# Performance work log

Measured on AMD Instinct MI355X. Metric: run time of the kernel, lower is better.

## Reference

```python
import jax, jax.numpy as jnp
import numpy as np

DIM = 1024
HEADS = 16
HEAD_DIM = DIM // HEADS
SCALE = HEAD_DIM ** -0.5


def setup_inputs() -> dict:
    key = jax.random.key(0)
    ks = jax.random.split(key, 7)
    B, N, M = 2, 2048, 2048
    x = jax.random.normal(ks[0], (B, N, DIM), dtype=jnp.float32)
    y = jax.random.normal(ks[1], (B, M, DIM), dtype=jnp.float32)
    s = DIM ** -0.5
    Wq = jax.random.normal(ks[2], (DIM, DIM), dtype=jnp.float32) * s
    Wk = jax.random.normal(ks[3], (DIM, DIM), dtype=jnp.float32) * s
    Wv = jax.random.normal(ks[4], (DIM, DIM), dtype=jnp.float32) * s
    Wp = jax.random.normal(ks[5], (DIM, DIM), dtype=jnp.float32) * s
    bp = jax.random.normal(ks[6], (DIM,), dtype=jnp.float32) * 0.01
    return {"x": x, "y": y, "Wq": Wq, "Wk": Wk, "Wv": Wv, "Wp": Wp, "bp": bp}


def _split_heads(t):
    b, n, _ = t.shape
    return t.reshape(b, n, HEADS, HEAD_DIM).transpose(0, 2, 1, 3)  # b h n d


def reference(x, y, Wq, Wk, Wv, Wp, bp):
    q = _split_heads(x @ Wq)  # [b,h,n,d]
    k = _split_heads(y @ Wk)  # [b,h,m,d]
    v = _split_heads(y @ Wv)  # [b,h,m,d]
    attn = jnp.einsum('bhid,bhjd->bhij', q, k) * SCALE  # [b,h,n,m]
    attn = jax.nn.softmax(attn, axis=-1)
    out = jnp.einsum('bhij,bhjd->bhid', attn, v)  # [b,h,n,d]
    b, h, n, d = out.shape
    out = out.transpose(0, 2, 1, 3).reshape(b, n, h * d)  # [b,n,dim]
    return out @ Wp + bp
```

## Files before the change

kernel.cpp:

```cpp
#include <hip/hip_runtime.h>
#include <hip/hip_bf16.h>
#include <cstdint>

#define DIM   1024
#define HEADS 16
#define HDIM  64
#define BATCH 2
#define SEQ   2048
#define ROWS  (BATCH*SEQ)
static constexpr float QSCALE = 0.18033688f;

typedef float  f32x4  __attribute__((ext_vector_type(4)));
typedef float  float4v __attribute__((ext_vector_type(4)));
typedef __bf16 bf16x8 __attribute__((ext_vector_type(8)));
typedef __bf16 bf16x4 __attribute__((ext_vector_type(4)));
typedef short  short4v __attribute__((ext_vector_type(4)));

#if __has_builtin(__builtin_amdgcn_mfma_f32_16x16x16_bf16)
__device__ __forceinline__ f32x4 mfma16(bf16x4 a, bf16x4 b, f32x4 c) {
  return __builtin_amdgcn_mfma_f32_16x16x16_bf16(a, b, c, 0, 0, 0);
}
#else
__device__ __forceinline__ f32x4 mfma16(bf16x4 a, bf16x4 b, f32x4 c) {
  return __builtin_amdgcn_mfma_f32_16x16x16bf16_1k(
      __builtin_bit_cast(short4v, a), __builtin_bit_cast(short4v, b), c, 0, 0, 0);
}
#endif

__device__ __forceinline__ void glds16(const __bf16* g, __bf16* l) {
  __builtin_amdgcn_global_load_lds(
      (const __attribute__((address_space(1))) void*)g,
      (__attribute__((address_space(3))) void*)l, 16, 0, 0);
}

__global__ __launch_bounds__(256) void prep_kernel(
    const float* __restrict__ x, const float* __restrict__ y,
    const float* __restrict__ Wq, const float* __restrict__ Wk,
    const float* __restrict__ Wv, const float* __restrict__ Wp,
    __bf16* __restrict__ xb, __bf16* __restrict__ yb, __bf16* __restrict__ Wt) {
  const int z = blockIdx.z, t = threadIdx.x;
  const size_t NEL = (size_t)ROWS * DIM;
  if (z < 8) {
    size_t idx = (((size_t)z * 1024 + blockIdx.x) * 256 + t) * 4;
    const float* s; __bf16* d;
    if (idx < NEL) { s = x + idx; d = xb + idx; }
    else           { s = y + (idx - NEL); d = yb + (idx - NEL); }
    const float4v v = *(const float4v*)s;
    bf16x4 o;
    o[0] = (__bf16)v[0]; o[1] = (__bf16)v[1]; o[2] = (__bf16)v[2]; o[3] = (__bf16)v[3];
    *(bf16x4*)d = o;
    return;
  }
  const int w = blockIdx.x >> 8, rem = blockIdx.x & 255;
  const float* W = (w == 0) ? Wq : (w == 1) ? Wk : (w == 2) ? Wv : Wp;
  __bf16* dst = Wt + (size_t)w * DIM * DIM;
  const int n0 = (rem & 15) * 64, k0 = (rem >> 4) * 64;
  __shared__ float T[64][65];
  const int col = t & 63, rw = t >> 6;
  #pragma unroll
  for (int p = 0; p < 16; ++p) {
    const int row = p * 4 + rw;
    T[row][col] = W[(size_t)(k0 + row) * DIM + n0 + col];
  }
  __syncthreads();
  #pragma unroll
  for (int p = 0; p < 16; ++p) {
    const int row = p * 4 + rw;
    dst[(size_t)(n0 + row) * DIM + k0 + col] = (__bf16)T[col][row];
  }
}

__global__ __launch_bounds__(256) void proj_kernel(
    const __bf16* __restrict__ xb, const __bf16* __restrict__ yb,
    const __bf16* __restrict__ Wt,
    __bf16* __restrict__ Qb, __bf16* __restrict__ Kb, __bf16* __restrict__ VT) {
  const int z = blockIdx.z;
  const __bf16* A = (z == 0) ? xb : yb;
  const __bf16* B = Wt + (size_t)z * DIM * DIM;

  __shared__ __bf16 As[128 * 64];
  __shared__ __bf16 Bs[128 * 64];

  const int t = threadIdx.x, lane = t & 63, wave = t >> 6;
  const int l15 = lane & 15, quad = lane >> 4;
  const int wm = wave & 1, wn = wave >> 1;
  const int rowBase = blockIdx.y * 128, colBase = blockIdx.x * 128;
  const int srow = lane >> 3;
  const int scol = ((lane & 7) ^ srow) * 8;

  f32x4 acc[4][4] = {};

  for (int kb = 0; kb < DIM; kb += 64) {
    __syncthreads();
    #pragma unroll
    for (int i = 0; i < 4; ++i) {
      const int c = wave * 4 + i;
      const int row = c * 8 + srow;
      glds16(&A[(size_t)(rowBase + row) * DIM + kb + scol], &As[c * 512]);
      glds16(&B[(size_t)(colBase + row) * DIM + kb + scol], &Bs[c * 512]);
    }
    __syncthreads();
    #pragma unroll
    for (int ks = 0; ks < 2; ++ks) {
      bf16x8 a[4], b[4];
      #pragma unroll
      for (int mi = 0; mi < 4; ++mi) {
        const int row = wm * 64 + mi * 16 + l15;
        a[mi] = *(const bf16x8*)&As[row * 64 + (((ks << 2) | quad) ^ (row & 7)) * 8];
      }
      #pragma unroll
      for (int ni = 0; ni < 4; ++ni) {
        const int row = wn * 64 + ni * 16 + l15;
        b[ni] = *(const bf16x8*)&Bs[row * 64 + (((ks << 2) | quad) ^ (row & 7)) * 8];
      }
      #pragma unroll
      for (int mi = 0; mi < 4; ++mi)
        #pragma unroll
        for (int ni = 0; ni < 4; ++ni)
          acc[mi][ni] = __builtin_amdgcn_mfma_f32_16x16x32_bf16(a[mi], b[ni], acc[mi][ni], 0, 0, 0);
    }
  }

  if (z < 2) {
    __bf16* out = (z == 0) ? Qb : Kb;
    const float sc = (z == 0) ? QSCALE : 1.0f;
    #pragma unroll
    for (int mi = 0; mi < 4; ++mi) {
      const int row0 = rowBase + wm * 64 + mi * 16 + quad * 4;
      #pragma unroll
      for (int ni = 0; ni < 4; ++ni) {
        const int col = colBase + wn * 64 + ni * 16 + l15;
        #pragma unroll
        for (int r = 0; r < 4; ++r)
          out[(size_t)(row0 + r) * DIM + col] = (__bf16)(acc[mi][ni][r] * sc);
      }
    }
  } else {
    #pragma unroll
    for (int mi = 0; mi < 4; ++mi) {
      const int row0 = rowBase + wm * 64 + mi * 16 + quad * 4;
      const int bb = row0 >> 11, key0 = row0 & (SEQ - 1);
      #pragma unroll
      for (int ni = 0; ni < 4; ++ni) {
        const int col = colBase + wn * 64 + ni * 16 + l15;
        const int h = col >> 6, d = col & 63;
        bf16x4 pk;
        #pragma unroll
        for (int r = 0; r < 4; ++r) pk[r] = (__bf16)acc[mi][ni][r];
        *(bf16x4*)&VT[((size_t)((bb * HEADS + h) * HDIM + d)) * SEQ + key0] = pk;
      }
    }
  }
}

__global__ __launch_bounds__(256, 2) void attn_kernel(
    const __bf16* __restrict__ Qb, const __bf16* __restrict__ Kb,
    const __bf16* __restrict__ VT, __bf16* __restrict__ Ob) {
  __shared__ __bf16 KV[2][2][64 * 64];
  __shared__ float lb[2][128];

  const int t = threadIdx.x, lane = t & 63, wave = t >> 6;
  const int l15 = lane & 15, quad = lane >> 4;
  const int bh = blockIdx.y, b = bh >> 4, h = bh & 15;
  const int qseg = wave & 1, kh = wave >> 1;
  const int qrow0 = blockIdx.x * 128 + qseg * 64;
  const int srow = lane >> 3;
  const int scol = ((lane & 7) ^ srow) * 8;

  const __bf16* Kbh = Kb + (size_t)b * SEQ * DIM + h * HDIM;
  const __bf16* Vbh = VT + (size_t)bh * HDIM * SEQ;

  bf16x8 qf[4][2];
  #pragma unroll
  for (int mi = 0; mi < 4; ++mi)
    #pragma unroll
    for (int ks = 0; ks < 2; ++ks)
      qf[mi][ks] = *(const bf16x8*)&Qb[(size_t)(b * SEQ + qrow0 + mi * 16 + l15) * DIM
                                       + h * HDIM + ks * 32 + quad * 8];

  f32x4 o[4][4] = {};
  float lsum[4] = {};

  auto stage = [&](int jb, int buf) {
    #pragma unroll
    for (int i = 0; i < 2; ++i) {
      const int c = wave * 2 + i;
      const int row = c * 8 + srow;
      glds16(&Kbh[(size_t)(jb + row) * DIM + scol], &KV[buf][0][c * 512]);
      glds16(&Vbh[(size_t)row * SEQ + jb + scol], &KV[buf][1][c * 512]);
    }
  };

  stage(0, 0);
  for (int j = 0; j < SEQ / 64; ++j) {
    const int buf = j & 1;
    __syncthreads();
    if (j + 1 < SEQ / 64) stage((j + 1) * 64, buf ^ 1);
    const __bf16* Ks = KV[buf][0];
    const __bf16* Vs = KV[buf][1];

    f32x4 sT[2][4] = {};
    #pragma unroll
    for (int ks = 0; ks < 2; ++ks)
      #pragma unroll
      for (int ni = 0; ni < 2; ++ni) {
        const int key = kh * 32 + ni * 16 + l15;
        const bf16x8 kf = *(const bf16x8*)&Ks[key * 64 + (((ks << 2) | quad) ^ (key & 7)) * 8];
        #pragma unroll
        for (int mi = 0; mi < 4; ++mi)
          sT[ni][mi] = __builtin_amdgcn_mfma_f32_16x16x32_bf16(kf, qf[mi][ks], sT[ni][mi], 0, 0, 0);
      }

    bf16x4 pa[2][4];
    #pragma unroll
    for (int ni = 0; ni < 2; ++ni)
      #pragma unroll
      for (int mi = 0; mi < 4; ++mi)
        #pragma unroll
        for (int r = 0; r < 4; ++r) {
          const float pv = __builtin_amdgcn_exp2f(sT[ni][mi][r]);
          lsum[mi] += pv;
          pa[ni][mi][r] = (__bf16)pv;
        }

    #pragma unroll
    for (int ni = 0; ni < 2; ++ni) {
      const int key0 = kh * 32 + ni * 16;
      #pragma unroll
      for (int dt = 0; dt < 4; ++dt) {
        const int d = dt * 16 + l15;
        const bf16x4 vf = *(const bf16x4*)&Vs[d * 64
            + (((key0 >> 3) + (quad >> 1)) ^ (d & 7)) * 8 + (quad & 1) * 4];
        #pragma unroll
        for (int mi = 0; mi < 4; ++mi)
          o[mi][dt] = mfma16(pa[ni][mi], vf, o[mi][dt]);
      }
    }
  }

  #pragma unroll
  for (int mi = 0; mi < 4; ++mi) {
    lsum[mi] += __shfl_xor(lsum[mi], 16, 64);
    lsum[mi] += __shfl_xor(lsum[mi], 32, 64);
  }
  __syncthreads();
  float* mb = (float*)&KV[0][0][0];
  if (quad == 0) {
    #pragma unroll
    for (int mi = 0; mi < 4; ++mi)
      lb[kh][qseg * 64 + mi * 16 + l15] = lsum[mi];
  }
  if (kh == 1) {
    #pragma unroll
    for (int mi = 0; mi < 4; ++mi)
      #pragma unroll
      for (int r = 0; r < 4; ++r) {
        const int q = mi * 16 + quad * 4 + r;
        #pragma unroll
        for (int dt = 0; dt < 4; ++dt)
          mb[qseg * 4096 + q * 64 + dt * 16 + l15] = o[mi][dt][r];
      }
  }
  __syncthreads();
  if (kh == 0) {
    #pragma unroll
    for (int mi = 0; mi < 4; ++mi)
      #pragma unroll
      for (int r = 0; r < 4; ++r) {
        const int q = mi * 16 + quad * 4 + r;
        const float inv = 1.f / (lb[0][qseg * 64 + q] + lb[1][qseg * 64 + q]);
        const size_t row = (size_t)(b * SEQ + qrow0 + q);
        #pragma unroll
        for (int dt = 0; dt < 4; ++dt) {
          const float ov = o[mi][dt][r] + mb[qseg * 4096 + q * 64 + dt * 16 + l15];
          Ob[row * DIM + h * HDIM + dt * 16 + l15] = (__bf16)(ov * inv);
        }
      }
  }
}

__global__ __launch_bounds__(256) void outproj_kernel(
    const __bf16* __restrict__ A, const __bf16* __restrict__ Bt,
    const float* __restrict__ bias, float* __restrict__ out) {
  __shared__ __bf16 As[128 * 64];
  __shared__ __bf16 Bs[128 * 64];

  const int t = threadIdx.x, lane = t & 63, wave = t >> 6;
  const int l15 = lane & 15, quad = lane >> 4;
  const int wm = wave & 1, wn = wave >> 1;
  const int rowBase = blockIdx.y * 128, colBase = blockIdx.x * 128;
  const int srow = lane >> 3;
  const int scol = ((lane & 7) ^ srow) * 8;

  f32x4 acc[4][4] = {};

  for (int kb = 0; kb < DIM; kb += 64) {
    __syncthreads();
    #pragma unroll
    for (int i = 0; i < 4; ++i) {
      const int c = wave * 4 + i;
      const int row = c * 8 + srow;
      glds16(&A[(size_t)(rowBase + row) * DIM + kb + scol], &As[c * 512]);
      glds16(&Bt[(size_t)(colBase + row) * DIM + kb + scol], &Bs[c * 512]);
    }
    __syncthreads();
    #pragma unroll
    for (int ks = 0; ks < 2; ++ks) {
      bf16x8 a[4], b[4];
      #pragma unroll
      for (int mi = 0; mi < 4; ++mi) {
        const int row = wm * 64 + mi * 16 + l15;
        a[mi] = *(const bf16x8*)&As[row * 64 + (((ks << 2) | quad) ^ (row & 7)) * 8];
      }
      #pragma unroll
      for (int ni = 0; ni < 4; ++ni) {
        const int row = wn * 64 + ni * 16 + l15;
        b[ni] = *(const bf16x8*)&Bs[row * 64 + (((ks << 2) | quad) ^ (row & 7)) * 8];
      }
      #pragma unroll
      for (int mi = 0; mi < 4; ++mi)
        #pragma unroll
        for (int ni = 0; ni < 4; ++ni)
          acc[mi][ni] = __builtin_amdgcn_mfma_f32_16x16x32_bf16(a[mi], b[ni], acc[mi][ni], 0, 0, 0);
    }
  }

  #pragma unroll
  for (int mi = 0; mi < 4; ++mi) {
    const int row0 = rowBase + wm * 64 + mi * 16 + quad * 4;
    #pragma unroll
    for (int ni = 0; ni < 4; ++ni) {
      const int col = colBase + wn * 64 + ni * 16 + l15;
      const float bb = bias[col];
      #pragma unroll
      for (int r = 0; r < 4; ++r)
        out[(size_t)(row0 + r) * DIM + col] = acc[mi][ni][r] + bb;
    }
  }
}

extern "C" void kernel_launch(void* const* d_in, const int* in_sizes, int n_in,
                              void* d_out, int out_size, void* d_ws, size_t ws_size,
                              hipStream_t stream) {
  const float* x  = (const float*)d_in[0];
  const float* y  = (const float*)d_in[1];
  const float* Wq = (const float*)d_in[2];
  const float* Wk = (const float*)d_in[3];
  const float* Wv = (const float*)d_in[4];
  const float* Wp = (const float*)d_in[5];
  const float* bp = (const float*)d_in[6];
  float* out = (float*)d_out;

  const size_t NEL = (size_t)ROWS * DIM;
  __bf16* xb = (__bf16*)d_ws;
  __bf16* yb = xb + NEL;
  __bf16* Wt = yb + NEL;
  __bf16* Qb = Wt + NEL;
  __bf16* Kb = Qb + NEL;
  __bf16* VT = Kb + NEL;
  __bf16* Ob = VT + NEL;

  prep_kernel<<<dim3(1024, 1, 9), 256, 0, stream>>>(x, y, Wq, Wk, Wv, Wp, xb, yb, Wt);
  proj_kernel<<<dim3(DIM / 128, ROWS / 128, 3), 256, 0, stream>>>(xb, yb, Wt, Qb, Kb, VT);
  attn_kernel<<<dim3(SEQ / 128, BATCH * HEADS), 256, 0, stream>>>(Qb, Kb, VT, Ob);
  outproj_kernel<<<dim3(DIM / 128, ROWS / 128), 256, 0, stream>>>(Ob, Wt + 3 * (size_t)DIM * DIM, bp, out);
}
```

Before: 214.1 us.

## Transpose V projection output through LDS and halve out-projection row tile

Splits the fused QKV projection into separate Q/K GEMM launches and a dedicated V projection kernel. The V kernel stages its tile through swizzled LDS so the transposed VT layout is written with coalesced 16-byte stores instead of scattered 8-byte ones. The output projection uses 64-row tiles to double the block count and improve CU fill. The attention output buffer reuses the x workspace. Extra launches remove the concurrency of the single z-grid launch.

```diff
diff --git a/kernel.cpp b/kernel.cpp
--- a/kernel.cpp
+++ b/kernel.cpp
@@ -70,14 +70,9 @@
   }
 }
 
-__global__ __launch_bounds__(256) void proj_kernel(
-    const __bf16* __restrict__ xb, const __bf16* __restrict__ yb,
-    const __bf16* __restrict__ Wt,
-    __bf16* __restrict__ Qb, __bf16* __restrict__ Kb, __bf16* __restrict__ VT) {
-  const int z = blockIdx.z;
-  const __bf16* A = (z == 0) ? xb : yb;
-  const __bf16* B = Wt + (size_t)z * DIM * DIM;
-
+__global__ __launch_bounds__(256) void gemm_bt_kernel(
+    const __bf16* __restrict__ A, const __bf16* __restrict__ Bt,
+    __bf16* __restrict__ out, float scale) {
   __shared__ __bf16 As[128 * 64];
   __shared__ __bf16 Bs[128 * 64];
 
@@ -97,7 +92,7 @@
       const int c = wave * 4 + i;
       const int row = c * 8 + srow;
       glds16(&A[(size_t)(rowBase + row) * DIM + kb + scol], &As[c * 512]);
-      glds16(&B[(size_t)(colBase + row) * DIM + kb + scol], &Bs[c * 512]);
+      glds16(&Bt[(size_t)(colBase + row) * DIM + kb + scol], &Bs[c * 512]);
     }
     __syncthreads();
     #pragma unroll
@@ -121,35 +116,90 @@
     }
   }
 
-  if (z < 2) {
-    __bf16* out = (z == 0) ? Qb : Kb;
-    const float sc = (z == 0) ? QSCALE : 1.0f;
-    #pragma unroll
-    for (int mi = 0; mi < 4; ++mi) {
-      const int row0 = rowBase + wm * 64 + mi * 16 + quad * 4;
+  #pragma unroll
+  for (int mi = 0; mi < 4; ++mi) {
+    const int row0 = rowBase + wm * 64 + mi * 16 + quad * 4;
+    #pragma unroll
+    for (int ni = 0; ni < 4; ++ni) {
+      const int col = colBase + wn * 64 + ni * 16 + l15;
+      #pragma unroll
+      for (int r = 0; r < 4; ++r)
+        out[(size_t)(row0 + r) * DIM + col] = (__bf16)(acc[mi][ni][r] * scale);
+    }
+  }
+}
+
+__global__ __launch_bounds__(256) void vproj_kernel(
+    const __bf16* __restrict__ A, const __bf16* __restrict__ Bt,
+    __bf16* __restrict__ VT) {
+  __shared__ __bf16 S[2][128 * 64];
+  __bf16* As = S[0];
+  __bf16* Bs = S[1];
+
+  const int t = threadIdx.x, lane = t & 63, wave = t >> 6;
+  const int l15 = lane & 15, quad = lane >> 4;
+  const int wm = wave & 1, wn = wave >> 1;
+  const int rowBase = blockIdx.y * 128, colBase = blockIdx.x * 128;
+  const int srow = lane >> 3;
+  const int scol = ((lane & 7) ^ srow) * 8;
+
+  f32x4 acc[4][4] = {};
+
+  for (int kb = 0; kb < DIM; kb += 64) {
+    __syncthreads();
+    #pragma unroll
+    for (int i = 0; i < 4; ++i) {
+      const int c = wave * 4 + i;
+      const int row = c * 8 + srow;
+      glds16(&A[(size_t)(rowBase + row) * DIM + kb + scol], &As[c * 512]);
+      glds16(&Bt[(size_t)(colBase + row) * DIM + kb + scol], &Bs[c * 512]);
+    }
+    __syncthreads();
+    #pragma unroll
+    for (int ks = 0; ks < 2; ++ks) {
+      bf16x8 a[4], b[4];
+      #pragma unroll
+      for (int mi = 0; mi < 4; ++mi) {
+        const int row = wm * 64 + mi * 16 + l15;
+        a[mi] = *(const bf16x8*)&As[row * 64 + (((ks << 2) | quad) ^ (row & 7)) * 8];
+      }
       #pragma unroll
       for (int ni = 0; ni < 4; ++ni) {
-        const int col = colBase + wn * 64 + ni * 16 + l15;
-        #pragma unroll
-        for (int r = 0; r < 4; ++r)
-          out[(size_t)(row0 + r) * DIM + col] = (__bf16)(acc[mi][ni][r] * sc);
-      }
-    }
-  } else {
-    #pragma unroll
-    for (int mi = 0; mi < 4; ++mi) {
-      const int row0 = rowBase + wm * 64 + mi * 16 + quad * 4;
-      const int bb = row0 >> 11, key0 = row0 & (SEQ - 1);
-      #pragma unroll
-      for (int ni = 0; ni < 4; ++ni) {
-        const int col = colBase + wn * 64 + ni * 16 + l15;
-        const int h = col >> 6, d = col & 63;
-        bf16x4 pk;
-        #pragma unroll
-        for (int r = 0; r < 4; ++r) pk[r] = (__bf16)acc[mi][ni][r];
-        *(bf16x4*)&VT[((size_t)((bb * HEADS + h) * HDIM + d)) * SEQ + key0] = pk;
-      }
-    }
+        const int row = wn * 64 + ni * 16 + l15;
+        b[ni] = *(const bf16x8*)&Bs[row * 64 + (((ks << 2) | quad) ^ (row & 7)) * 8];
+      }
+      #pragma unroll
+      for (int mi = 0; mi < 4; ++mi)
+        #pragma unroll
+        for (int ni = 0; ni < 4; ++ni)
+          acc[mi][ni] = __builtin_amdgcn_mfma_f32_16x16x32_bf16(a[mi], b[ni], acc[mi][ni], 0, 0, 0);
+    }
+  }
+
+  __syncthreads();
+  __bf16* Ts = &S[0][0];
+  #pragma unroll
+  for (int mi = 0; mi < 4; ++mi) {
+    const int bk3 = wm * 8 + mi * 2 + (quad >> 1);
+    #pragma unroll
+    for (int ni = 0; ni < 4; ++ni) {
+      const int dl = wn * 64 + ni * 16 + l15;
+      bf16x4 pk;
+      #pragma unroll
+      for (int r = 0; r < 4; ++r) pk[r] = (__bf16)acc[mi][ni][r];
+      *(bf16x4*)&Ts[dl * 128 + (bk3 ^ (dl & 7)) * 8 + (quad & 1) * 4] = pk;
+    }
+  }
+  __syncthreads();
+  const int d = t >> 1, khh = t & 1;
+  const size_t vrow = (size_t)((rowBase >> 11) * HEADS * HDIM) + colBase + d;
+  const int key0g = rowBase & (SEQ - 1);
+  #pragma unroll
+  for (int j = 0; j < 8; ++j) {
+    const int kc = khh * 8 + j;
+    const int lc = (kc & 8) | ((kc ^ d) & 7);
+    const bf16x8 v = *(const bf16x8*)&Ts[d * 128 + lc * 8];
+    *(bf16x8*)&VT[vrow * SEQ + key0g + kc * 8] = v;
   }
 }
 
@@ -282,34 +332,39 @@
 __global__ __launch_bounds__(256) void outproj_kernel(
     const __bf16* __restrict__ A, const __bf16* __restrict__ Bt,
     const float* __restrict__ bias, float* __restrict__ out) {
-  __shared__ __bf16 As[128 * 64];
+  __shared__ __bf16 As[64 * 64];
   __shared__ __bf16 Bs[128 * 64];
 
   const int t = threadIdx.x, lane = t & 63, wave = t >> 6;
   const int l15 = lane & 15, quad = lane >> 4;
   const int wm = wave & 1, wn = wave >> 1;
-  const int rowBase = blockIdx.y * 128, colBase = blockIdx.x * 128;
+  const int rowBase = blockIdx.y * 64, colBase = blockIdx.x * 128;
   const int srow = lane >> 3;
   const int scol = ((lane & 7) ^ srow) * 8;
 
-  f32x4 acc[4][4] = {};
+  f32x4 acc[2][4] = {};
 
   for (int kb = 0; kb < DIM; kb += 64) {
     __syncthreads();
+    #pragma unroll
+    for (int i = 0; i < 2; ++i) {
+      const int c = wave * 2 + i;
+      const int row = c * 8 + srow;
+      glds16(&A[(size_t)(rowBase + row) * DIM + kb + scol], &As[c * 512]);
+    }
     #pragma unroll
     for (int i = 0; i < 4; ++i) {
       const int c = wave * 4 + i;
       const int row = c * 8 + srow;
-      glds16(&A[(size_t)(rowBase + row) * DIM + kb + scol], &As[c * 512]);
       glds16(&Bt[(size_t)(colBase + row) * DIM + kb + scol], &Bs[c * 512]);
     }
     __syncthreads();
     #pragma unroll
     for (int ks = 0; ks < 2; ++ks) {
-      bf16x8 a[4], b[4];
-      #pragma unroll
-      for (int mi = 0; mi < 4; ++mi) {
-        const int row = wm * 64 + mi * 16 + l15;
+      bf16x8 a[2], b[4];
+      #pragma unroll
+      for (int mi = 0; mi < 2; ++mi) {
+        const int row = wm * 32 + mi * 16 + l15;
         a[mi] = *(const bf16x8*)&As[row * 64 + (((ks << 2) | quad) ^ (row & 7)) * 8];
       }
       #pragma unroll
@@ -318,7 +373,7 @@
         b[ni] = *(const bf16x8*)&Bs[row * 64 + (((ks << 2) | quad) ^ (row & 7)) * 8];
       }
       #pragma unroll
-      for (int mi = 0; mi < 4; ++mi)
+      for (int mi = 0; mi < 2; ++mi)
         #pragma unroll
         for (int ni = 0; ni < 4; ++ni)
           acc[mi][ni] = __builtin_amdgcn_mfma_f32_16x16x32_bf16(a[mi], b[ni], acc[mi][ni], 0, 0, 0);
@@ -326,8 +381,8 @@
   }
 
   #pragma unroll
-  for (int mi = 0; mi < 4; ++mi) {
-    const int row0 = rowBase + wm * 64 + mi * 16 + quad * 4;
+  for (int mi = 0; mi < 2; ++mi) {
+    const int row0 = rowBase + wm * 32 + mi * 16 + quad * 4;
     #pragma unroll
     for (int ni = 0; ni < 4; ++ni) {
       const int col = colBase + wn * 64 + ni * 16 + l15;
@@ -358,10 +413,12 @@
   __bf16* Qb = Wt + NEL;
   __bf16* Kb = Qb + NEL;
   __bf16* VT = Kb + NEL;
-  __bf16* Ob = VT + NEL;
+  __bf16* Ob = xb;
 
   prep_kernel<<<dim3(1024, 1, 9), 256, 0, stream>>>(x, y, Wq, Wk, Wv, Wp, xb, yb, Wt);
-  proj_kernel<<<dim3(DIM / 128, ROWS / 128, 3), 256, 0, stream>>>(xb, yb, Wt, Qb, Kb, VT);
+  gemm_bt_kernel<<<dim3(DIM / 128, ROWS / 128), 256, 0, stream>>>(xb, Wt, Qb, QSCALE);
+  gemm_bt_kernel<<<dim3(DIM / 128, ROWS / 128), 256, 0, stream>>>(yb, Wt + NEL / 4, Kb, 1.0f);
+  vproj_kernel<<<dim3(DIM / 128, ROWS / 128), 256, 0, stream>>>(yb, Wt + NEL / 2, VT);
   attn_kernel<<<dim3(SEQ / 128, BATCH * HEADS), 256, 0, stream>>>(Qb, Kb, VT, Ob);
-  outproj_kernel<<<dim3(DIM / 128, ROWS / 128), 256, 0, stream>>>(Ob, Wt + 3 * (size_t)DIM * DIM, bp, out);
-}
+  outproj_kernel<<<dim3(DIM / 128, ROWS / 64), 256, 0, stream>>>(Ob, Wt + 3 * NEL / 4, bp, out);
+}
```

Result: slower. 230.9 us (+7.8%).
